# Kernel tuning notes

Hardware: AMD Instinct MI355X
Metric: run time of the kernel (lower is better)

Reference implementation:

```python
import jax, jax.numpy as jnp
import numpy as np

B, N, D = 16, 2048, 128

def setup_inputs() -> dict:
    key = jax.random.key(0)
    kq, kk, kv = jax.random.split(key, 3)
    q = jax.random.normal(kq, (B, N, D), dtype=jnp.float32)
    k = jax.random.normal(kk, (B, N, D), dtype=jnp.float32)
    v = jax.random.normal(kv, (B, N, D), dtype=jnp.float32)
    return {"q": q, "k": k, "v": v}

def reference(q, k, v):
    # attn = softmax(q @ k^T, axis=2)   (NOTE: no temperature scaling, matching source)
    scores = jnp.einsum("bnd,bmd->bnm", q, k)  # [B, N, N]
    attn = jax.nn.softmax(scores, axis=2)
    # dropout p=0.0 -> identity
    output = jnp.einsum("bnm,bmd->bnd", attn, v)  # [B, N, D]
    return (output, attn)
```

## Files before the change

kernel.cpp:

```cpp
#include <hip/hip_runtime.h>

#define N 2048
#define D 128
#define BB 16

typedef __attribute__((ext_vector_type(8))) short s16x8;
typedef __attribute__((ext_vector_type(4))) float f32x4;

__device__ __forceinline__ void split2(float x0, float x1, unsigned& h, unsigned& l) {
    unsigned b0 = __float_as_uint(x0), b1 = __float_as_uint(x1);
    float r0 = x0 - __uint_as_float(b0 & 0xffff0000u);
    float r1 = x1 - __uint_as_float(b1 & 0xffff0000u);
    h = (b0 >> 16) | (b1 & 0xffff0000u);
    l = (__float_as_uint(r0) >> 16) | (__float_as_uint(r1) & 0xffff0000u);
}

__device__ __forceinline__ s16x8 pack16(uint4 u) {
    union { uint4 a; s16x8 b; } x; x.a = u; return x.b;
}

__global__ __launch_bounds__(256) void zero_kernel(float4* __restrict__ p, int n4) {
    int i = blockIdx.x * 256 + threadIdx.x;
    const int stride = gridDim.x * 256;
    for (; i < n4; i += stride) p[i] = make_float4(0.f, 0.f, 0.f, 0.f);
}

__global__ __launch_bounds__(256) void vt_kernel(const float* __restrict__ v,
                                                 unsigned short* __restrict__ vth,
                                                 unsigned short* __restrict__ vtl) {
    const int t    = threadIdx.x;
    const int lane = t & 63;
    const int w    = t >> 6;
    const int b    = blockIdx.z;
    const int n0   = blockIdx.x * 32 + w * 8;
    const int d    = blockIdx.y * 64 + lane;
    const float* vp = v + ((size_t)b * N + n0) * D + d;
    float x[8];
    #pragma unroll
    for (int i = 0; i < 8; ++i) x[i] = vp[(size_t)i * D];
    uint4 h, l;
    split2(x[0], x[1], h.x, l.x);
    split2(x[2], x[3], h.y, l.y);
    split2(x[4], x[5], h.z, l.z);
    split2(x[6], x[7], h.w, l.w);
    size_t idx = ((size_t)b * D + d) * N + n0;
    *(uint4*)(vth + idx) = h;
    *(uint4*)(vtl + idx) = l;
}

__global__ __launch_bounds__(256) void qs_kernel(const float* __restrict__ q,
                                                 const float* __restrict__ k,
                                                 float* __restrict__ outp) {
    __shared__ unsigned short Qh[128 * 32], Ql[128 * 32];
    __shared__ unsigned short Kh[128 * 32], Kl[128 * 32];
    const int t  = threadIdx.x;
    const int b  = blockIdx.z;
    const int ib = blockIdx.y * 128;
    const int jb = blockIdx.x * 128;
    const float* qp = q + ((size_t)b * N + ib) * D;
    const float* kp = k + ((size_t)b * N + jb) * D;

    const int lane = t & 63;
    const int w    = t >> 6;
    const int wr   = (w >> 1) * 64;
    const int wc   = (w & 1) * 64;
    const int l15  = lane & 15;
    const int l4   = lane >> 4;

    f32x4 acc[4][4] = {};

    for (int ks = 0; ks < 4; ++ks) {
        __syncthreads();
        #pragma unroll
        for (int c = 0; c < 4; ++c) {
            int flat = c * 256 + t;
            int row  = flat >> 3;
            int f4   = flat & 7;
            float4 qv = *(const float4*)(qp + (size_t)row * D + ks * 32 + f4 * 4);
            float4 kv = *(const float4*)(kp + (size_t)row * D + ks * 32 + f4 * 4);
            int idx = row * 32 + (((f4 >> 1) ^ (row & 3)) * 8) + (f4 & 1) * 4;
            uint2 hh, ll;
            split2(qv.x, qv.y, hh.x, ll.x);
            split2(qv.z, qv.w, hh.y, ll.y);
            *(uint2*)(Qh + idx) = hh;
            *(uint2*)(Ql + idx) = ll;
            split2(kv.x, kv.y, hh.x, ll.x);
            split2(kv.z, kv.w, hh.y, ll.y);
            *(uint2*)(Kh + idx) = hh;
            *(uint2*)(Kl + idx) = ll;
        }
        __syncthreads();

        s16x8 ah[4], al[4], bh[4], bl[4];
        #pragma unroll
        for (int ti = 0; ti < 4; ++ti) {
            int row = wr + ti * 16 + l15;
            int idx = row * 32 + ((l4 ^ (row & 3)) * 8);
            ah[ti] = *(const s16x8*)(Qh + idx);
            al[ti] = *(const s16x8*)(Ql + idx);
        }
        #pragma unroll
        for (int tj = 0; tj < 4; ++tj) {
            int row = wc + tj * 16 + l15;
            int idx = row * 32 + ((l4 ^ (row & 3)) * 8);
            bh[tj] = *(const s16x8*)(Kh + idx);
            bl[tj] = *(const s16x8*)(Kl + idx);
        }
        #pragma unroll
        for (int ti = 0; ti < 4; ++ti)
            #pragma unroll
            for (int tj = 0; tj < 4; ++tj) {
                acc[ti][tj] = __builtin_amdgcn_mfma_f32_16x16x32_bf16(ah[ti], bh[tj], acc[ti][tj], 0, 0, 0);
                acc[ti][tj] = __builtin_amdgcn_mfma_f32_16x16x32_bf16(ah[ti], bl[tj], acc[ti][tj], 0, 0, 0);
                acc[ti][tj] = __builtin_amdgcn_mfma_f32_16x16x32_bf16(al[ti], bh[tj], acc[ti][tj], 0, 0, 0);
            }
    }

    #pragma unroll
    for (int ti = 0; ti < 4; ++ti) {
        #pragma unroll
        for (int r = 0; r < 4; ++r) {
            int row = ib + wr + ti * 16 + l4 * 4 + r;
            float rs = 0.f;
            #pragma unroll
            for (int tj = 0; tj < 4; ++tj) rs += __expf(acc[ti][tj][r]);
            rs += __shfl_xor(rs, 1);
            rs += __shfl_xor(rs, 2);
            rs += __shfl_xor(rs, 4);
            rs += __shfl_xor(rs, 8);
            if (l15 == 0) atomicAdd(outp + ((size_t)b * N + row) * D, rs);
        }
    }
}

__global__ __launch_bounds__(256, 2) void fused_kernel(const float* __restrict__ q,
                                                       const float* __restrict__ k,
                                                       const unsigned short* __restrict__ vth,
                                                       const unsigned short* __restrict__ vtl,
                                                       float* __restrict__ attn,
                                                       float* __restrict__ outp) {
    __shared__ unsigned short Kh[64 * 128], Kl[64 * 128];
    __shared__ unsigned short Vh[128 * 64], Vl[128 * 64];
    float* Pf = (float*)Kh;

    const int t = threadIdx.x, lane = t & 63, w = t >> 6;
    const int b = blockIdx.y, ib = blockIdx.x * 64;
    const int l15 = lane & 15, l4 = lane >> 4;
    const float* qp = q + ((size_t)b * N + ib) * D;
    const float* kp = k + (size_t)b * N * D;
    const unsigned short* vhp = vth + (size_t)b * D * N;
    const unsigned short* vlp = vtl + (size_t)b * D * N;
    float* ap = attn + ((size_t)b * N + ib) * N;
    float* op = outp + ((size_t)b * N + ib) * D;

    float inv[4];
    #pragma unroll
    for (int r = 0; r < 4; ++r)
        inv[r] = 1.0f / op[(size_t)(w * 16 + l4 * 4 + r) * D];

    s16x8 qh[4], ql[4];
    {
        const float* qrow = qp + (size_t)(w * 16 + l15) * D;
        #pragma unroll
        for (int ks = 0; ks < 4; ++ks) {
            float4 x0 = *(const float4*)(qrow + ks * 32 + l4 * 8);
            float4 x1 = *(const float4*)(qrow + ks * 32 + l4 * 8 + 4);
            uint4 h, l;
            split2(x0.x, x0.y, h.x, l.x);
            split2(x0.z, x0.w, h.y, l.y);
            split2(x1.x, x1.y, h.z, l.z);
            split2(x1.z, x1.w, h.w, l.w);
            qh[ks] = pack16(h);
            ql[ks] = pack16(l);
        }
    }

    f32x4 oacc[8] = {};

    float4 kf[8];
    uint4 fh[4], fl[4];
    #pragma unroll
    for (int c = 0; c < 8; ++c) {
        int flat4 = c * 256 + t;
        int row = flat4 >> 5, f4 = flat4 & 31;
        kf[c] = *(const float4*)(kp + (size_t)row * D + f4 * 4);
    }
    #pragma unroll
    for (int c = 0; c < 4; ++c) {
        int flat = c * 256 + t;
        int d = flat >> 3, g = flat & 7;
        fh[c] = *(const uint4*)(vhp + (size_t)d * N + g * 8);
        fl[c] = *(const uint4*)(vlp + (size_t)d * N + g * 8);
    }

    for (int jc = 0; jc < 32; ++jc) {
        __syncthreads();
        #pragma unroll
        for (int c = 0; c < 8; ++c) {
            int flat4 = c * 256 + t;
            int row = flat4 >> 5, f4 = flat4 & 31;
            uint2 hh, ll;
            split2(kf[c].x, kf[c].y, hh.x, ll.x);
            split2(kf[c].z, kf[c].w, hh.y, ll.y);
            int idx = row * 128 + (((f4 >> 1) ^ (row & 7)) * 8) + (f4 & 1) * 4;
            *(uint2*)(Kh + idx) = hh;
            *(uint2*)(Kl + idx) = ll;
        }
        #pragma unroll
        for (int c = 0; c < 4; ++c) {
            int flat = c * 256 + t;
            int d = flat >> 3, g = flat & 7;
            int idx = d * 64 + ((g ^ (d & 7)) * 8);
            *(uint4*)(Vh + idx) = fh[c];
            *(uint4*)(Vl + idx) = fl[c];
        }
        __syncthreads();
        if (jc < 31) {
            #pragma unroll
            for (int c = 0; c < 8; ++c) {
                int flat4 = c * 256 + t;
                int row = flat4 >> 5, f4 = flat4 & 31;
                kf[c] = *(const float4*)(kp + (size_t)((jc + 1) * 64 + row) * D + f4 * 4);
            }
            #pragma unroll
            for (int c = 0; c < 4; ++c) {
                int flat = c * 256 + t;
                int d = flat >> 3, g = flat & 7;
                fh[c] = *(const uint4*)(vhp + (size_t)d * N + (jc + 1) * 64 + g * 8);
                fl[c] = *(const uint4*)(vlp + (size_t)d * N + (jc + 1) * 64 + g * 8);
            }
        }
        f32x4 sacc[4] = {};
        #pragma unroll
        for (int ks = 0; ks < 4; ++ks) {
            s16x8 bh[4], bl[4];
            #pragma unroll
            for (int tj = 0; tj < 4; ++tj) {
                int row = tj * 16 + l15;
                int idx = row * 128 + (((ks * 4 + l4) ^ (row & 7)) * 8);
                bh[tj] = *(const s16x8*)(Kh + idx);
                bl[tj] = *(const s16x8*)(Kl + idx);
            }
            #pragma unroll
            for (int tj = 0; tj < 4; ++tj) {
                sacc[tj] = __builtin_amdgcn_mfma_f32_16x16x32_bf16(qh[ks], bh[tj], sacc[tj], 0, 0, 0);
                sacc[tj] = __builtin_amdgcn_mfma_f32_16x16x32_bf16(qh[ks], bl[tj], sacc[tj], 0, 0, 0);
                sacc[tj] = __builtin_amdgcn_mfma_f32_16x16x32_bf16(ql[ks], bh[tj], sacc[tj], 0, 0, 0);
            }
        }
        __syncthreads();
        float* pw = Pf + w * (16 * 64);
        #pragma unroll
        for (int r = 0; r < 4; ++r) {
            int row = l4 * 4 + r;
            float* arow = ap + (size_t)(w * 16 + row) * N + jc * 64;
            #pragma unroll
            for (int tj = 0; tj < 4; ++tj) {
                float pv = __expf(sacc[tj][r]) * inv[r];
                arow[tj * 16 + l15] = pv;
                int gw = (tj * 4 + (l15 >> 2)) ^ ((row & 7) << 1);
                pw[row * 64 + gw * 4 + (l15 & 3)] = pv;
            }
        }
        #pragma unroll
        for (int ks2 = 0; ks2 < 2; ++ks2) {
            int g0 = (ks2 * 8 + l4 * 2) ^ ((l15 & 7) << 1);
            float4 p0 = *(const float4*)(pw + l15 * 64 + g0 * 4);
            float4 p1 = *(const float4*)(pw + l15 * 64 + g0 * 4 + 4);
            uint4 h, l;
            split2(p0.x, p0.y, h.x, l.x);
            split2(p0.z, p0.w, h.y, l.y);
            split2(p1.x, p1.y, h.z, l.z);
            split2(p1.z, p1.w, h.w, l.w);
            s16x8 pah = pack16(h), pal = pack16(l);
            #pragma unroll
            for (int df = 0; df < 8; ++df) {
                int dr = df * 16 + l15;
                int idx = dr * 64 + (((ks2 * 4 + l4) ^ (dr & 7)) * 8);
                s16x8 vbh = *(const s16x8*)(Vh + idx);
                s16x8 vbl = *(const s16x8*)(Vl + idx);
                oacc[df] = __builtin_amdgcn_mfma_f32_16x16x32_bf16(pah, vbh, oacc[df], 0, 0, 0);
                oacc[df] = __builtin_amdgcn_mfma_f32_16x16x32_bf16(pah, vbl, oacc[df], 0, 0, 0);
                oacc[df] = __builtin_amdgcn_mfma_f32_16x16x32_bf16(pal, vbh, oacc[df], 0, 0, 0);
            }
        }
    }

    #pragma unroll
    for (int r = 0; r < 4; ++r) {
        int row = w * 16 + l4 * 4 + r;
        #pragma unroll
        for (int df = 0; df < 8; ++df)
            op[(size_t)row * D + df * 16 + l15] = oacc[df][r];
    }
}

__global__ __launch_bounds__(256) void qk_kernel(const float* __restrict__ q,
                                                 const float* __restrict__ k,
                                                 float* __restrict__ attn,
                                                 float* __restrict__ outp) {
    __shared__ unsigned short Qh[128 * 32], Ql[128 * 32];
    __shared__ unsigned short Kh[128 * 32], Kl[128 * 32];
    const int t  = threadIdx.x;
    const int b  = blockIdx.z;
    const int ib = blockIdx.y * 128;
    const int jb = blockIdx.x * 128;
    const float* qp = q + ((size_t)b * N + ib) * D;
    const float* kp = k + ((size_t)b * N + jb) * D;

    const int lane = t & 63;
    const int w    = t >> 6;
    const int wr   = (w >> 1) * 64;
    const int wc   = (w & 1) * 64;
    const int l15  = lane & 15;
    const int l4   = lane >> 4;

    f32x4 acc[4][4] = {};

    for (int ks = 0; ks < 4; ++ks) {
        __syncthreads();
        #pragma unroll
        for (int c = 0; c < 4; ++c) {
            int flat = c * 256 + t;
            int row  = flat >> 3;
            int f4   = flat & 7;
            float4 qv = *(const float4*)(qp + (size_t)row * D + ks * 32 + f4 * 4);
            float4 kv = *(const float4*)(kp + (size_t)row * D + ks * 32 + f4 * 4);
            int idx = row * 32 + (((f4 >> 1) ^ (row & 3)) * 8) + (f4 & 1) * 4;
            uint2 hh, ll;
            split2(qv.x, qv.y, hh.x, ll.x);
            split2(qv.z, qv.w, hh.y, ll.y);
            *(uint2*)(Qh + idx) = hh;
            *(uint2*)(Ql + idx) = ll;
            split2(kv.x, kv.y, hh.x, ll.x);
            split2(kv.z, kv.w, hh.y, ll.y);
            *(uint2*)(Kh + idx) = hh;
            *(uint2*)(Kl + idx) = ll;
        }
        __syncthreads();

        s16x8 ah[4], al[4], bh[4], bl[4];
        #pragma unroll
        for (int ti = 0; ti < 4; ++ti) {
            int row = wr + ti * 16 + l15;
            int idx = row * 32 + ((l4 ^ (row & 3)) * 8);
            ah[ti] = *(const s16x8*)(Qh + idx);
            al[ti] = *(const s16x8*)(Ql + idx);
        }
        #pragma unroll
        for (int tj = 0; tj < 4; ++tj) {
            int row = wc + tj * 16 + l15;
            int idx = row * 32 + ((l4 ^ (row & 3)) * 8);
            bh[tj] = *(const s16x8*)(Kh + idx);
            bl[tj] = *(const s16x8*)(Kl + idx);
        }
        #pragma unroll
        for (int ti = 0; ti < 4; ++ti)
            #pragma unroll
            for (int tj = 0; tj < 4; ++tj) {
                acc[ti][tj] = __builtin_amdgcn_mfma_f32_16x16x32_bf16(ah[ti], bh[tj], acc[ti][tj], 0, 0, 0);
                acc[ti][tj] = __builtin_amdgcn_mfma_f32_16x16x32_bf16(ah[ti], bl[tj], acc[ti][tj], 0, 0, 0);
                acc[ti][tj] = __builtin_amdgcn_mfma_f32_16x16x32_bf16(al[ti], bh[tj], acc[ti][tj], 0, 0, 0);
            }
    }

    #pragma unroll
    for (int ti = 0; ti < 4; ++ti) {
        #pragma unroll
        for (int r = 0; r < 4; ++r) {
            int row = ib + wr + ti * 16 + l4 * 4 + r;
            float* arow = attn + ((size_t)b * N + row) * N + jb + wc;
            float rs = 0.f;
            #pragma unroll
            for (int tj = 0; tj < 4; ++tj) {
                float e = __expf(acc[ti][tj][r]);
                arow[tj * 16 + l15] = e;
                rs += e;
            }
            rs += __shfl_xor(rs, 1);
            rs += __shfl_xor(rs, 2);
            rs += __shfl_xor(rs, 4);
            rs += __shfl_xor(rs, 8);
            if (l15 == 0) atomicAdd(outp + ((size_t)b * N + row) * D, rs);
        }
    }
}

__global__ __launch_bounds__(256) void pv_fb_kernel(const float* __restrict__ v,
                                                    float* __restrict__ attn,
                                                    float* __restrict__ outp) {
    __shared__ unsigned short Ph[64 * 64], Pl[64 * 64];
    __shared__ unsigned short Vth[128 * 64], Vtl[128 * 64];
    __shared__ float invs[64];
    const int t  = threadIdx.x;
    const int b  = blockIdx.y;
    const int ib = blockIdx.x * 64;
    float* ap       = attn + ((size_t)b * N + ib) * N;
    const float* vp = v + (size_t)b * N * D;
    float* op       = outp + ((size_t)b * N + ib) * D;

    if (t < 64) invs[t] = 1.0f / op[(size_t)t * D];

    const int lane = t & 63;
    const int w    = t >> 6;
    const int rg   = (w >> 1) * 32;
    const int dg   = (w & 1) * 64;
    const int l15  = lane & 15;
    const int l4   = lane >> 4;

    f32x4 acc[2][4] = {};

    float4 pe[4], va[4], vb[4];
    #pragma unroll
    for (int c = 0; c < 4; ++c) {
        int flat = c * 256 + t;
        pe[c] = *(const float4*)(ap + (size_t)(flat >> 4) * N + (flat & 15) * 4);
        int jp = flat >> 5, d4 = flat & 31;
        va[c] = *(const float4*)(vp + (size_t)(jp * 2) * D + d4 * 4);
        vb[c] = *(const float4*)(vp + (size_t)(jp * 2 + 1) * D + d4 * 4);
    }

    for (int jc = 0; jc < 32; ++jc) {
        __syncthreads();
        #pragma unroll
        for (int c = 0; c < 4; ++c) {
            int flat = c * 256 + t;
            int row = flat >> 4, j4 = flat & 15;
            float iv = invs[row];
            float4 p4;
            p4.x = pe[c].x * iv; p4.y = pe[c].y * iv;
            p4.z = pe[c].z * iv; p4.w = pe[c].w * iv;
            *(float4*)(ap + (size_t)row * N + jc * 64 + j4 * 4) = p4;
            uint2 hh, ll;
            split2(p4.x, p4.y, hh.x, ll.x);
            split2(p4.z, p4.w, hh.y, ll.y);
            int idx = row * 64 + (((j4 >> 1) ^ (row & 7)) * 8) + (j4 & 1) * 4;
            *(uint2*)(Ph + idx) = hh;
            *(uint2*)(Pl + idx) = ll;
        }
        #pragma unroll
        for (int c = 0; c < 4; ++c) {
            int flat = c * 256 + t;
            int jp = flat >> 5, d4 = flat & 31;
            int j = jp * 2;
            float4 v0 = va[c], v1 = vb[c];
            #pragma unroll
            for (int e = 0; e < 4; ++e) {
                float x0 = (&v0.x)[e], x1 = (&v1.x)[e];
                unsigned h, l;
                split2(x0, x1, h, l);
                int d = d4 * 4 + e;
                int idx = d * 64 + (((j >> 3) ^ (d & 7)) * 8) + (j & 7);
                *(unsigned*)(Vth + idx) = h;
                *(unsigned*)(Vtl + idx) = l;
            }
        }
        __syncthreads();
        if (jc < 31) {
            #pragma unroll
            for (int c = 0; c < 4; ++c) {
                int flat = c * 256 + t;
                pe[c] = *(const float4*)(ap + (size_t)(flat >> 4) * N + (jc + 1) * 64 + (flat & 15) * 4);
                int jp = flat >> 5, d4 = flat & 31;
                va[c] = *(const float4*)(vp + (size_t)((jc + 1) * 64 + jp * 2) * D + d4 * 4);
                vb[c] = *(const float4*)(vp + (size_t)((jc + 1) * 64 + jp * 2 + 1) * D + d4 * 4);
            }
        }
        #pragma unroll
        for (int ksj = 0; ksj < 2; ++ksj) {
            s16x8 pah[2], pal[2], bh[4], bl[4];
            #pragma unroll
            for (int ti = 0; ti < 2; ++ti) {
                int row = rg + ti * 16 + l15;
                int idx = row * 64 + (((ksj * 4 + l4) ^ (row & 7)) * 8);
                pah[ti] = *(const s16x8*)(Ph + idx);
                pal[ti] = *(const s16x8*)(Pl + idx);
            }
            #pragma unroll
            for (int tj = 0; tj < 4; ++tj) {
                int d = dg + tj * 16 + l15;
                int idx = d * 64 + (((ksj * 4 + l4) ^ (d & 7)) * 8);
                bh[tj] = *(const s16x8*)(Vth + idx);
                bl[tj] = *(const s16x8*)(Vtl + idx);
            }
            #pragma unroll
            for (int ti = 0; ti < 2; ++ti)
                #pragma unroll
                for (int tj = 0; tj < 4; ++tj) {
                    acc[ti][tj] = __builtin_amdgcn_mfma_f32_16x16x32_bf16(pah[ti], bh[tj], acc[ti][tj], 0, 0, 0);
                    acc[ti][tj] = __builtin_amdgcn_mfma_f32_16x16x32_bf16(pah[ti], bl[tj], acc[ti][tj], 0, 0, 0);
                    acc[ti][tj] = __builtin_amdgcn_mfma_f32_16x16x32_bf16(pal[ti], bh[tj], acc[ti][tj], 0, 0, 0);
                }
        }
    }

    #pragma unroll
    for (int ti = 0; ti < 2; ++ti)
        #pragma unroll
        for (int r = 0; r < 4; ++r) {
            int row = rg + ti * 16 + l4 * 4 + r;
            #pragma unroll
            for (int tj = 0; tj < 4; ++tj)
                op[(size_t)row * D + dg + tj * 16 + l15] = acc[ti][tj][r];
        }
}

extern "C" void kernel_launch(void* const* d_in, const int* in_sizes, int n_in,
                              void* d_out, int out_size, void* d_ws, size_t ws_size,
                              hipStream_t stream) {
    const float* q = (const float*)d_in[0];
    const float* k = (const float*)d_in[1];
    const float* v = (const float*)d_in[2];
    float* out  = (float*)d_out;
    float* attn = out + (size_t)BB * N * D;

    const size_t vt_elems = (size_t)BB * D * N;
    const bool use_ws = ws_size >= vt_elems * 2 * sizeof(unsigned short);

    zero_kernel<<<1024, 256, 0, stream>>>((float4*)out, BB * N * D / 4);
    if (use_ws) {
        unsigned short* vth = (unsigned short*)d_ws;
        unsigned short* vtl = vth + vt_elems;
        vt_kernel<<<dim3(N / 32, 2, BB), 256, 0, stream>>>(v, vth, vtl);
        qs_kernel<<<dim3(N / 128, N / 128, BB), 256, 0, stream>>>(q, k, out);
        fused_kernel<<<dim3(N / 64, BB), 256, 0, stream>>>(q, k, vth, vtl, attn, out);
    } else {
        qk_kernel<<<dim3(N / 128, N / 128, BB), 256, 0, stream>>>(q, k, attn, out);
        pv_fb_kernel<<<dim3(N / 64, BB), 256, 0, stream>>>(v, attn, out);
    }
}
```

Baseline: 568.1 us.

## Restructure row-sum pass per row block and stage attention stores through LDS

The row-sum kernel changes from a 2D tiled grid with atomicAdd into one block per 64-row query tile. Each block loops over all K chunks, accumulates row sums in registers and writes them directly, so the zero-fill kernel is no longer needed on this path. The fused kernel now writes attention probabilities through the LDS tile as coalesced float4 stores instead of scattered scalar stores. The cost is a longer serial loop per block with fewer blocks, which may lower parallelism in the row-sum pass.

```diff
diff --git a/kernel.cpp b/kernel.cpp
--- a/kernel.cpp
+++ b/kernel.cpp
@@ -48,8 +48,280 @@
     *(uint4*)(vtl + idx) = l;
 }
 
-__global__ __launch_bounds__(256) void qs_kernel(const float* __restrict__ q,
+__global__ __launch_bounds__(256, 2) void qs_kernel(const float* __restrict__ q,
+                                                    const float* __restrict__ k,
+                                                    float* __restrict__ outp) {
+    __shared__ unsigned short Qh[64 * 128], Ql[64 * 128];
+    __shared__ unsigned short Kh[64 * 128], Kl[64 * 128];
+    const int t = threadIdx.x, lane = t & 63, w = t >> 6;
+    const int b = blockIdx.y, ib = blockIdx.x * 64;
+    const int l15 = lane & 15, l4 = lane >> 4;
+    const float* qp = q + ((size_t)b * N + ib) * D;
+    const float* kp = k + (size_t)b * N * D;
+
+    #pragma unroll
+    for (int c = 0; c < 8; ++c) {
+        int flat4 = c * 256 + t;
+        int row = flat4 >> 5, f4 = flat4 & 31;
+        float4 qv = *(const float4*)(qp + (size_t)row * D + f4 * 4);
+        uint2 hh, ll;
+        split2(qv.x, qv.y, hh.x, ll.x);
+        split2(qv.z, qv.w, hh.y, ll.y);
+        int idx = row * 128 + (((f4 >> 1) ^ (row & 7)) * 8) + (f4 & 1) * 4;
+        *(uint2*)(Qh + idx) = hh;
+        *(uint2*)(Ql + idx) = ll;
+    }
+    __syncthreads();
+    s16x8 qh[4], ql[4];
+    {
+        int row = w * 16 + l15;
+        #pragma unroll
+        for (int ks = 0; ks < 4; ++ks) {
+            int idx = row * 128 + (((ks * 4 + l4) ^ (row & 7)) * 8);
+            qh[ks] = *(const s16x8*)(Qh + idx);
+            ql[ks] = *(const s16x8*)(Ql + idx);
+        }
+    }
+
+    float rs[4] = {0.f, 0.f, 0.f, 0.f};
+
+    float4 kf[8];
+    #pragma unroll
+    for (int c = 0; c < 8; ++c) {
+        int flat4 = c * 256 + t;
+        int row = flat4 >> 5, f4 = flat4 & 31;
+        kf[c] = *(const float4*)(kp + (size_t)row * D + f4 * 4);
+    }
+
+    for (int jc = 0; jc < 32; ++jc) {
+        __syncthreads();
+        #pragma unroll
+        for (int c = 0; c < 8; ++c) {
+            int flat4 = c * 256 + t;
+            int row = flat4 >> 5, f4 = flat4 & 31;
+            uint2 hh, ll;
+            split2(kf[c].x, kf[c].y, hh.x, ll.x);
+            split2(kf[c].z, kf[c].w, hh.y, ll.y);
+            int idx = row * 128 + (((f4 >> 1) ^ (row & 7)) * 8) + (f4 & 1) * 4;
+            *(uint2*)(Kh + idx) = hh;
+            *(uint2*)(Kl + idx) = ll;
+        }
+        __syncthreads();
+        if (jc < 31) {
+            #pragma unroll
+            for (int c = 0; c < 8; ++c) {
+                int flat4 = c * 256 + t;
+                int row = flat4 >> 5, f4 = flat4 & 31;
+                kf[c] = *(const float4*)(kp + (size_t)((jc + 1) * 64 + row) * D + f4 * 4);
+            }
+        }
+        f32x4 sacc[4] = {};
+        #pragma unroll
+        for (int ks = 0; ks < 4; ++ks) {
+            s16x8 bh[4], bl[4];
+            #pragma unroll
+            for (int tj = 0; tj < 4; ++tj) {
+                int row = tj * 16 + l15;
+                int idx = row * 128 + (((ks * 4 + l4) ^ (row & 7)) * 8);
+                bh[tj] = *(const s16x8*)(Kh + idx);
+                bl[tj] = *(const s16x8*)(Kl + idx);
+            }
+            #pragma unroll
+            for (int tj = 0; tj < 4; ++tj) {
+                sacc[tj] = __builtin_amdgcn_mfma_f32_16x16x32_bf16(qh[ks], bh[tj], sacc[tj], 0, 0, 0);
+                sacc[tj] = __builtin_amdgcn_mfma_f32_16x16x32_bf16(qh[ks], bl[tj], sacc[tj], 0, 0, 0);
+                sacc[tj] = __builtin_amdgcn_mfma_f32_16x16x32_bf16(ql[ks], bh[tj], sacc[tj], 0, 0, 0);
+            }
+        }
+        #pragma unroll
+        for (int r = 0; r < 4; ++r)
+            #pragma unroll
+            for (int tj = 0; tj < 4; ++tj) rs[r] += __expf(sacc[tj][r]);
+    }
+
+    #pragma unroll
+    for (int r = 0; r < 4; ++r) {
+        float v0 = rs[r];
+        v0 += __shfl_xor(v0, 1);
+        v0 += __shfl_xor(v0, 2);
+        v0 += __shfl_xor(v0, 4);
+        v0 += __shfl_xor(v0, 8);
+        if (l15 == 0)
+            outp[((size_t)b * N + ib + w * 16 + l4 * 4 + r) * D] = v0;
+    }
+}
+
+__global__ __launch_bounds__(256, 2) void fused_kernel(const float* __restrict__ q,
+                                                       const float* __restrict__ k,
+                                                       const unsigned short* __restrict__ vth,
+                                                       const unsigned short* __restrict__ vtl,
+                                                       float* __restrict__ attn,
+                                                       float* __restrict__ outp) {
+    __shared__ unsigned short Kh[64 * 128], Kl[64 * 128];
+    __shared__ unsigned short Vh[128 * 64], Vl[128 * 64];
+    float* Pf = (float*)Kh;
+
+    const int t = threadIdx.x, lane = t & 63, w = t >> 6;
+    const int b = blockIdx.y, ib = blockIdx.x * 64;
+    const int l15 = lane & 15, l4 = lane >> 4;
+    const float* qp = q + ((size_t)b * N + ib) * D;
+    const float* kp = k + (size_t)b * N * D;
+    const unsigned short* vhp = vth + (size_t)b * D * N;
+    const unsigned short* vlp = vtl + (size_t)b * D * N;
+    float* ap = attn + ((size_t)b * N + ib) * N;
+    float* op = outp + ((size_t)b * N + ib) * D;
+
+    float inv[4];
+    #pragma unroll
+    for (int r = 0; r < 4; ++r)
+        inv[r] = 1.0f / op[(size_t)(w * 16 + l4 * 4 + r) * D];
+
+    s16x8 qh[4], ql[4];
+    {
+        const float* qrow = qp + (size_t)(w * 16 + l15) * D;
+        #pragma unroll
+        for (int ks = 0; ks < 4; ++ks) {
+            float4 x0 = *(const float4*)(qrow + ks * 32 + l4 * 8);
+            float4 x1 = *(const float4*)(qrow + ks * 32 + l4 * 8 + 4);
+            uint4 h, l;
+            split2(x0.x, x0.y, h.x, l.x);
+            split2(x0.z, x0.w, h.y, l.y);
+            split2(x1.x, x1.y, h.z, l.z);
+            split2(x1.z, x1.w, h.w, l.w);
+            qh[ks] = pack16(h);
+            ql[ks] = pack16(l);
+        }
+    }
+
+    f32x4 oacc[8] = {};
+
+    float4 kf[8];
+    uint4 fh[4], fl[4];
+    #pragma unroll
+    for (int c = 0; c < 8; ++c) {
+        int flat4 = c * 256 + t;
+        int row = flat4 >> 5, f4 = flat4 & 31;
+        kf[c] = *(const float4*)(kp + (size_t)row * D + f4 * 4);
+    }
+    #pragma unroll
+    for (int c = 0; c < 4; ++c) {
+        int flat = c * 256 + t;
+        int d = flat >> 3, g = flat & 7;
+        fh[c] = *(const uint4*)(vhp + (size_t)d * N + g * 8);
+        fl[c] = *(const uint4*)(vlp + (size_t)d * N + g * 8);
+    }
+
+    for (int jc = 0; jc < 32; ++jc) {
+        __syncthreads();
+        #pragma unroll
+        for (int c = 0; c < 8; ++c) {
+            int flat4 = c * 256 + t;
+            int row = flat4 >> 5, f4 = flat4 & 31;
+            uint2 hh, ll;
+            split2(kf[c].x, kf[c].y, hh.x, ll.x);
+            split2(kf[c].z, kf[c].w, hh.y, ll.y);
+            int idx = row * 128 + (((f4 >> 1) ^ (row & 7)) * 8) + (f4 & 1) * 4;
+            *(uint2*)(Kh + idx) = hh;
+            *(uint2*)(Kl + idx) = ll;
+        }
+        #pragma unroll
+        for (int c = 0; c < 4; ++c) {
+            int flat = c * 256 + t;
+            int d = flat >> 3, g = flat & 7;
+            int idx = d * 64 + ((g ^ (d & 7)) * 8);
+            *(uint4*)(Vh + idx) = fh[c];
+            *(uint4*)(Vl + idx) = fl[c];
+        }
+        __syncthreads();
+        if (jc < 31) {
+            #pragma unroll
+            for (int c = 0; c < 8; ++c) {
+                int flat4 = c * 256 + t;
+                int row = flat4 >> 5, f4 = flat4 & 31;
+                kf[c] = *(const float4*)(kp + (size_t)((jc + 1) * 64 + row) * D + f4 * 4);
+            }
+            #pragma unroll
+            for (int c = 0; c < 4; ++c) {
+                int flat = c * 256 + t;
+                int d = flat >> 3, g = flat & 7;
+                fh[c] = *(const uint4*)(vhp + (size_t)d * N + (jc + 1) * 64 + g * 8);
+                fl[c] = *(const uint4*)(vlp + (size_t)d * N + (jc + 1) * 64 + g * 8);
+            }
+        }
+        f32x4 sacc[4] = {};
+        #pragma unroll
+        for (int ks = 0; ks < 4; ++ks) {
+            s16x8 bh[4], bl[4];
+            #pragma unroll
+            for (int tj = 0; tj < 4; ++tj) {
+                int row = tj * 16 + l15;
+                int idx = row * 128 + (((ks * 4 + l4) ^ (row & 7)) * 8);
+                bh[tj] = *(const s16x8*)(Kh + idx);
+                bl[tj] = *(const s16x8*)(Kl + idx);
+            }
+            #pragma unroll
+            for (int tj = 0; tj < 4; ++tj) {
+                sacc[tj] = __builtin_amdgcn_mfma_f32_16x16x32_bf16(qh[ks], bh[tj], sacc[tj], 0, 0, 0);
+                sacc[tj] = __builtin_amdgcn_mfma_f32_16x16x32_bf16(qh[ks], bl[tj], sacc[tj], 0, 0, 0);
+                sacc[tj] = __builtin_amdgcn_mfma_f32_16x16x32_bf16(ql[ks], bh[tj], sacc[tj], 0, 0, 0);
+            }
+        }
+        __syncthreads();
+        float* pw = Pf + w * (16 * 64);
+        #pragma unroll
+        for (int r = 0; r < 4; ++r) {
+            int row = l4 * 4 + r;
+            #pragma unroll
+            for (int tj = 0; tj < 4; ++tj) {
+                float pv = __expf(sacc[tj][r]) * inv[r];
+                int gw = (tj * 4 + (l15 >> 2)) ^ ((row & 7) << 1);
+                pw[row * 64 + gw * 4 + (l15 & 3)] = pv;
+            }
+        }
+        #pragma unroll
+        for (int m = 0; m < 4; ++m) {
+            int row = (m & 1) * 8 + (lane >> 3);
+            int lg  = (lane & 7) + (m >> 1) * 8;
+            int pg  = lg ^ ((row & 7) << 1);
+            float4 pv4 = *(const float4*)(pw + row * 64 + pg * 4);
+            *(float4*)(ap + (size_t)(w * 16 + row) * N + jc * 64 + lg * 4) = pv4;
+        }
+        #pragma unroll
+        for (int ks2 = 0; ks2 < 2; ++ks2) {
+            int g0 = (ks2 * 8 + l4 * 2) ^ ((l15 & 7) << 1);
+            float4 p0 = *(const float4*)(pw + l15 * 64 + g0 * 4);
+            float4 p1 = *(const float4*)(pw + l15 * 64 + g0 * 4 + 4);
+            uint4 h, l;
+            split2(p0.x, p0.y, h.x, l.x);
+            split2(p0.z, p0.w, h.y, l.y);
+            split2(p1.x, p1.y, h.z, l.z);
+            split2(p1.z, p1.w, h.w, l.w);
+            s16x8 pah = pack16(h), pal = pack16(l);
+            #pragma unroll
+            for (int df = 0; df < 8; ++df) {
+                int dr = df * 16 + l15;
+                int idx = dr * 64 + (((ks2 * 4 + l4) ^ (dr & 7)) * 8);
+                s16x8 vbh = *(const s16x8*)(Vh + idx);
+                s16x8 vbl = *(const s16x8*)(Vl + idx);
+                oacc[df] = __builtin_amdgcn_mfma_f32_16x16x32_bf16(pah, vbh, oacc[df], 0, 0, 0);
+                oacc[df] = __builtin_amdgcn_mfma_f32_16x16x32_bf16(pah, vbl, oacc[df], 0, 0, 0);
+                oacc[df] = __builtin_amdgcn_mfma_f32_16x16x32_bf16(pal, vbh, oacc[df], 0, 0, 0);
+            }
+        }
+    }
+
+    #pragma unroll
+    for (int r = 0; r < 4; ++r) {
+        int row = w * 16 + l4 * 4 + r;
+        #pragma unroll
+        for (int df = 0; df < 8; ++df)
+            op[(size_t)row * D + df * 16 + l15] = oacc[df][r];
+    }
+}
+
+__global__ __launch_bounds__(256) void qk_kernel(const float* __restrict__ q,
                                                  const float* __restrict__ k,
+                                                 float* __restrict__ attn,
                                                  float* __restrict__ outp) {
     __shared__ unsigned short Qh[128 * 32], Ql[128 * 32];
     __shared__ unsigned short Kh[128 * 32], Kl[128 * 32];
@@ -121,254 +393,6 @@
         #pragma unroll
         for (int r = 0; r < 4; ++r) {
             int row = ib + wr + ti * 16 + l4 * 4 + r;
-            float rs = 0.f;
-            #pragma unroll
-            for (int tj = 0; tj < 4; ++tj) rs += __expf(acc[ti][tj][r]);
-            rs += __shfl_xor(rs, 1);
-            rs += __shfl_xor(rs, 2);
-            rs += __shfl_xor(rs, 4);
-            rs += __shfl_xor(rs, 8);
-            if (l15 == 0) atomicAdd(outp + ((size_t)b * N + row) * D, rs);
-        }
-    }
-}
-
-__global__ __launch_bounds__(256, 2) void fused_kernel(const float* __restrict__ q,
-                                                       const float* __restrict__ k,
-                                                       const unsigned short* __restrict__ vth,
-                                                       const unsigned short* __restrict__ vtl,
-                                                       float* __restrict__ attn,
-                                                       float* __restrict__ outp) {
-    __shared__ unsigned short Kh[64 * 128], Kl[64 * 128];
-    __shared__ unsigned short Vh[128 * 64], Vl[128 * 64];
-    float* Pf = (float*)Kh;
-
-    const int t = threadIdx.x, lane = t & 63, w = t >> 6;
-    const int b = blockIdx.y, ib = blockIdx.x * 64;
-    const int l15 = lane & 15, l4 = lane >> 4;
-    const float* qp = q + ((size_t)b * N + ib) * D;
-    const float* kp = k + (size_t)b * N * D;
-    const unsigned short* vhp = vth + (size_t)b * D * N;
-    const unsigned short* vlp = vtl + (size_t)b * D * N;
-    float* ap = attn + ((size_t)b * N + ib) * N;
-    float* op = outp + ((size_t)b * N + ib) * D;
-
-    float inv[4];
-    #pragma unroll
-    for (int r = 0; r < 4; ++r)
-        inv[r] = 1.0f / op[(size_t)(w * 16 + l4 * 4 + r) * D];
-
-    s16x8 qh[4], ql[4];
-    {
-        const float* qrow = qp + (size_t)(w * 16 + l15) * D;
-        #pragma unroll
-        for (int ks = 0; ks < 4; ++ks) {
-            float4 x0 = *(const float4*)(qrow + ks * 32 + l4 * 8);
-            float4 x1 = *(const float4*)(qrow + ks * 32 + l4 * 8 + 4);
-            uint4 h, l;
-            split2(x0.x, x0.y, h.x, l.x);
-            split2(x0.z, x0.w, h.y, l.y);
-            split2(x1.x, x1.y, h.z, l.z);
-            split2(x1.z, x1.w, h.w, l.w);
-            qh[ks] = pack16(h);
-            ql[ks] = pack16(l);
-        }
-    }
-
-    f32x4 oacc[8] = {};
-
-    float4 kf[8];
-    uint4 fh[4], fl[4];
-    #pragma unroll
-    for (int c = 0; c < 8; ++c) {
-        int flat4 = c * 256 + t;
-        int row = flat4 >> 5, f4 = flat4 & 31;
-        kf[c] = *(const float4*)(kp + (size_t)row * D + f4 * 4);
-    }
-    #pragma unroll
-    for (int c = 0; c < 4; ++c) {
-        int flat = c * 256 + t;
-        int d = flat >> 3, g = flat & 7;
-        fh[c] = *(const uint4*)(vhp + (size_t)d * N + g * 8);
-        fl[c] = *(const uint4*)(vlp + (size_t)d * N + g * 8);
-    }
-
-    for (int jc = 0; jc < 32; ++jc) {
-        __syncthreads();
-        #pragma unroll
-        for (int c = 0; c < 8; ++c) {
-            int flat4 = c * 256 + t;
-            int row = flat4 >> 5, f4 = flat4 & 31;
-            uint2 hh, ll;
-            split2(kf[c].x, kf[c].y, hh.x, ll.x);
-            split2(kf[c].z, kf[c].w, hh.y, ll.y);
-            int idx = row * 128 + (((f4 >> 1) ^ (row & 7)) * 8) + (f4 & 1) * 4;
-            *(uint2*)(Kh + idx) = hh;
-            *(uint2*)(Kl + idx) = ll;
-        }
-        #pragma unroll
-        for (int c = 0; c < 4; ++c) {
-            int flat = c * 256 + t;
-            int d = flat >> 3, g = flat & 7;
-            int idx = d * 64 + ((g ^ (d & 7)) * 8);
-            *(uint4*)(Vh + idx) = fh[c];
-            *(uint4*)(Vl + idx) = fl[c];
-        }
-        __syncthreads();
-        if (jc < 31) {
-            #pragma unroll
-            for (int c = 0; c < 8; ++c) {
-                int flat4 = c * 256 + t;
-                int row = flat4 >> 5, f4 = flat4 & 31;
-                kf[c] = *(const float4*)(kp + (size_t)((jc + 1) * 64 + row) * D + f4 * 4);
-            }
-            #pragma unroll
-            for (int c = 0; c < 4; ++c) {
-                int flat = c * 256 + t;
-                int d = flat >> 3, g = flat & 7;
-                fh[c] = *(const uint4*)(vhp + (size_t)d * N + (jc + 1) * 64 + g * 8);
-                fl[c] = *(const uint4*)(vlp + (size_t)d * N + (jc + 1) * 64 + g * 8);
-            }
-        }
-        f32x4 sacc[4] = {};
-        #pragma unroll
-        for (int ks = 0; ks < 4; ++ks) {
-            s16x8 bh[4], bl[4];
-            #pragma unroll
-            for (int tj = 0; tj < 4; ++tj) {
-                int row = tj * 16 + l15;
-                int idx = row * 128 + (((ks * 4 + l4) ^ (row & 7)) * 8);
-                bh[tj] = *(const s16x8*)(Kh + idx);
-                bl[tj] = *(const s16x8*)(Kl + idx);
-            }
-            #pragma unroll
-            for (int tj = 0; tj < 4; ++tj) {
-                sacc[tj] = __builtin_amdgcn_mfma_f32_16x16x32_bf16(qh[ks], bh[tj], sacc[tj], 0, 0, 0);
-                sacc[tj] = __builtin_amdgcn_mfma_f32_16x16x32_bf16(qh[ks], bl[tj], sacc[tj], 0, 0, 0);
-                sacc[tj] = __builtin_amdgcn_mfma_f32_16x16x32_bf16(ql[ks], bh[tj], sacc[tj], 0, 0, 0);
-            }
-        }
-        __syncthreads();
-        float* pw = Pf + w * (16 * 64);
-        #pragma unroll
-        for (int r = 0; r < 4; ++r) {
-            int row = l4 * 4 + r;
-            float* arow = ap + (size_t)(w * 16 + row) * N + jc * 64;
-            #pragma unroll
-            for (int tj = 0; tj < 4; ++tj) {
-                float pv = __expf(sacc[tj][r]) * inv[r];
-                arow[tj * 16 + l15] = pv;
-                int gw = (tj * 4 + (l15 >> 2)) ^ ((row & 7) << 1);
-                pw[row * 64 + gw * 4 + (l15 & 3)] = pv;
-            }
-        }
-        #pragma unroll
-        for (int ks2 = 0; ks2 < 2; ++ks2) {
-            int g0 = (ks2 * 8 + l4 * 2) ^ ((l15 & 7) << 1);
-            float4 p0 = *(const float4*)(pw + l15 * 64 + g0 * 4);
-            float4 p1 = *(const float4*)(pw + l15 * 64 + g0 * 4 + 4);
-            uint4 h, l;
-            split2(p0.x, p0.y, h.x, l.x);
-            split2(p0.z, p0.w, h.y, l.y);
-            split2(p1.x, p1.y, h.z, l.z);
-            split2(p1.z, p1.w, h.w, l.w);
-            s16x8 pah = pack16(h), pal = pack16(l);
-            #pragma unroll
-            for (int df = 0; df < 8; ++df) {
-                int dr = df * 16 + l15;
-                int idx = dr * 64 + (((ks2 * 4 + l4) ^ (dr & 7)) * 8);
-                s16x8 vbh = *(const s16x8*)(Vh + idx);
-                s16x8 vbl = *(const s16x8*)(Vl + idx);
-                oacc[df] = __builtin_amdgcn_mfma_f32_16x16x32_bf16(pah, vbh, oacc[df], 0, 0, 0);
-                oacc[df] = __builtin_amdgcn_mfma_f32_16x16x32_bf16(pah, vbl, oacc[df], 0, 0, 0);
-                oacc[df] = __builtin_amdgcn_mfma_f32_16x16x32_bf16(pal, vbh, oacc[df], 0, 0, 0);
-            }
-        }
-    }
-
-    #pragma unroll
-    for (int r = 0; r < 4; ++r) {
-        int row = w * 16 + l4 * 4 + r;
-        #pragma unroll
-        for (int df = 0; df < 8; ++df)
-            op[(size_t)row * D + df * 16 + l15] = oacc[df][r];
-    }
-}
-
-__global__ __launch_bounds__(256) void qk_kernel(const float* __restrict__ q,
-                                                 const float* __restrict__ k,
-                                                 float* __restrict__ attn,
-                                                 float* __restrict__ outp) {
-    __shared__ unsigned short Qh[128 * 32], Ql[128 * 32];
-    __shared__ unsigned short Kh[128 * 32], Kl[128 * 32];
-    const int t  = threadIdx.x;
-    const int b  = blockIdx.z;
-    const int ib = blockIdx.y * 128;
-    const int jb = blockIdx.x * 128;
-    const float* qp = q + ((size_t)b * N + ib) * D;
-    const float* kp = k + ((size_t)b * N + jb) * D;
-
-    const int lane = t & 63;
-    const int w    = t >> 6;
-    const int wr   = (w >> 1) * 64;
-    const int wc   = (w & 1) * 64;
-    const int l15  = lane & 15;
-    const int l4   = lane >> 4;
-
-    f32x4 acc[4][4] = {};
-
-    for (int ks = 0; ks < 4; ++ks) {
-        __syncthreads();
-        #pragma unroll
-        for (int c = 0; c < 4; ++c) {
-            int flat = c * 256 + t;
-            int row  = flat >> 3;
-            int f4   = flat & 7;
-            float4 qv = *(const float4*)(qp + (size_t)row * D + ks * 32 + f4 * 4);
-            float4 kv = *(const float4*)(kp + (size_t)row * D + ks * 32 + f4 * 4);
-            int idx = row * 32 + (((f4 >> 1) ^ (row & 3)) * 8) + (f4 & 1) * 4;
-            uint2 hh, ll;
-            split2(qv.x, qv.y, hh.x, ll.x);
-            split2(qv.z, qv.w, hh.y, ll.y);
-            *(uint2*)(Qh + idx) = hh;
-            *(uint2*)(Ql + idx) = ll;
-            split2(kv.x, kv.y, hh.x, ll.x);
-            split2(kv.z, kv.w, hh.y, ll.y);
-            *(uint2*)(Kh + idx) = hh;
-            *(uint2*)(Kl + idx) = ll;
-        }
-        __syncthreads();
-
-        s16x8 ah[4], al[4], bh[4], bl[4];
-        #pragma unroll
-        for (int ti = 0; ti < 4; ++ti) {
-            int row = wr + ti * 16 + l15;
-            int idx = row * 32 + ((l4 ^ (row & 3)) * 8);
-            ah[ti] = *(const s16x8*)(Qh + idx);
-            al[ti] = *(const s16x8*)(Ql + idx);
-        }
-        #pragma unroll
-        for (int tj = 0; tj < 4; ++tj) {
-            int row = wc + tj * 16 + l15;
-            int idx = row * 32 + ((l4 ^ (row & 3)) * 8);
-            bh[tj] = *(const s16x8*)(Kh + idx);
-            bl[tj] = *(const s16x8*)(Kl + idx);
-        }
-        #pragma unroll
-        for (int ti = 0; ti < 4; ++ti)
-            #pragma unroll
-            for (int tj = 0; tj < 4; ++tj) {
-                acc[ti][tj] = __builtin_amdgcn_mfma_f32_16x16x32_bf16(ah[ti], bh[tj], acc[ti][tj], 0, 0, 0);
-                acc[ti][tj] = __builtin_amdgcn_mfma_f32_16x16x32_bf16(ah[ti], bl[tj], acc[ti][tj], 0, 0, 0);
-                acc[ti][tj] = __builtin_amdgcn_mfma_f32_16x16x32_bf16(al[ti], bh[tj], acc[ti][tj], 0, 0, 0);
-            }
-    }
-
-    #pragma unroll
-    for (int ti = 0; ti < 4; ++ti) {
-        #pragma unroll
-        for (int r = 0; r < 4; ++r) {
-            int row = ib + wr + ti * 16 + l4 * 4 + r;
             float* arow = attn + ((size_t)b * N + row) * N + jb + wc;
             float rs = 0.f;
             #pragma unroll
@@ -517,14 +541,14 @@
     const size_t vt_elems = (size_t)BB * D * N;
     const bool use_ws = ws_size >= vt_elems * 2 * sizeof(unsigned short);
 
-    zero_kernel<<<1024, 256, 0, stream>>>((float4*)out, BB * N * D / 4);
     if (use_ws) {
         unsigned short* vth = (unsigned short*)d_ws;
         unsigned short* vtl = vth + vt_elems;
         vt_kernel<<<dim3(N / 32, 2, BB), 256, 0, stream>>>(v, vth, vtl);
-        qs_kernel<<<dim3(N / 128, N / 128, BB), 256, 0, stream>>>(q, k, out);
+        qs_kernel<<<dim3(N / 64, BB), 256, 0, stream>>>(q, k, out);
         fused_kernel<<<dim3(N / 64, BB), 256, 0, stream>>>(q, k, vth, vtl, attn, out);
     } else {
+        zero_kernel<<<1024, 256, 0, stream>>>((float4*)out, BB * N * D / 4);
         qk_kernel<<<dim3(N / 128, N / 128, BB), 256, 0, stream>>>(q, k, attn, out);
         pv_fb_kernel<<<dim3(N / 64, BB), 256, 0, stream>>>(v, attn, out);
     }
```

Measured after the change: 514.8 us. -9.4%, faster.
